# Kernel tuning notes

Hardware: AMD Instinct MI355X
Metric: run time of the kernel (lower is better)

## Reference

```python
import jax, jax.numpy as jnp
import numpy as np

D = 512
EPS = 1e-5  # torch BatchNorm1d default eps


def swish(x):
    return x * jax.nn.sigmoid(x)


def batchnorm_train(x, gamma, beta):
    # BatchNorm1d in training mode: biased batch stats
    m = jnp.mean(x, axis=0)
    v = jnp.mean((x - m) ** 2, axis=0)
    return gamma * (x - m) / jnp.sqrt(v + EPS) + beta


def setup_inputs() -> dict:
    key = jax.random.key(0)
    k_fea, k_w1, k_w2, k_lerp = jax.random.split(key, 4)
    bs, P = 32768, 8192
    fea = jax.random.normal(k_fea, (bs, D), dtype=jnp.float32)
    # first P rows are the minority (positive) class
    lbl = jnp.concatenate([jnp.ones((P, 1), jnp.int32), jnp.zeros((bs - P, 1), jnp.int32)], axis=0)
    scale = 1.0 / np.sqrt(D)
    W1 = jax.random.normal(k_w1, (D, D), dtype=jnp.float32) * scale
    W2 = jax.random.normal(k_w2, (D, D), dtype=jnp.float32) * scale
    b1 = jnp.zeros((D,), jnp.float32)
    b2 = jnp.zeros((D,), jnp.float32)
    g1 = jnp.ones((D,), jnp.float32)
    g2 = jnp.ones((D,), jnp.float32)
    beta1 = jnp.zeros((D,), jnp.float32)
    beta2 = jnp.zeros((D,), jnp.float32)
    lerp_w = jax.random.uniform(k_lerp, (P, 3), dtype=jnp.float32)
    return dict(fea=fea, lbl=lbl, W1=W1, b1=b1, g1=g1, beta1=beta1,
                W2=W2, b2=b2, g2=g2, beta2=beta2, lerp_w=lerp_w, num_pos=P)


def reference(fea, lbl, W1, b1, g1, beta1, W2, b2, g2, beta2, lerp_w, num_pos):
    # fea_transform: Linear -> BN -> Swish -> Linear -> BN -> Swish
    h = swish(batchnorm_train(fea @ W1 + b1, g1, beta1))
    h = swish(batchnorm_train(h @ W2 + b2, g2, beta2))

    # SMOTE path (training mode): KNN over positive-class features
    pos_idx = jnp.nonzero(lbl[:, 0] > 0, size=num_pos)[0]  # static-size gather
    x = h[pos_idx]                                          # (P, D)
    sq = jnp.sum(x * x, axis=-1)                            # (P,)
    # negative squared pairwise distance; topk largest == nearest
    neg_dist = 2.0 * (x @ x.T) - sq[:, None] - sq[None, :]  # (P, P)
    _, idx = jax.lax.top_k(neg_dist, 3)                     # (P, 3), idx[:,0] == self

    a = x[idx[:, 0]]                                        # (P, D) anchor
    b = x[idx]                                              # (P, 3, D) neighbors
    # torch.lerp(a, b, w) = a + w * (b - a), one random w per (i, j)
    new_fea = a[:, None, :] + lerp_w[..., None] * (b - a[:, None, :])
    new_fea = new_fea.reshape(-1, D)                        # (3P, D), row-major matches i,j loop order

    fea_out = jnp.concatenate([h, new_fea], axis=0)
    lbl_out = jnp.concatenate([lbl, jnp.ones((new_fea.shape[0], 1), lbl.dtype)], axis=0)
    return fea_out, lbl_out
```

## Files before the change

### kernel.cpp

```cpp
#include <hip/hip_runtime.h>
#include <math.h>

#define NEG_INF -3.402823466e38f
#define NSPLIT 8

typedef __attribute__((ext_vector_type(8))) short bf16x8;
typedef __attribute__((ext_vector_type(4))) float f32x4;

__device__ __forceinline__ void gload_lds16(const unsigned short* g, unsigned short* l) {
  __builtin_amdgcn_global_load_lds(
      (const __attribute__((address_space(1))) unsigned int*)g,
      (__attribute__((address_space(3))) unsigned int*)l, 16, 0, 0);
}
__device__ __forceinline__ void gload_lds16f(const float* g, float* l) {
  __builtin_amdgcn_global_load_lds(
      (const __attribute__((address_space(1))) unsigned int*)g,
      (__attribute__((address_space(3))) unsigned int*)l, 16, 0, 0);
}

__device__ __forceinline__ unsigned short f2bf(float f) {
  union { float f; unsigned int u; } a; a.f = f;
  unsigned int u = a.u;
  return (unsigned short)((u + 0x7fffu + ((u >> 16) & 1u)) >> 16);
}

__device__ __forceinline__ void split3_8(f32x4 a, f32x4 b,
                                         bf16x8& hi, bf16x8& md, bf16x8& lo) {
  union { bf16x8 v; unsigned int u[4]; } H, M, L;
  float f[8];
  f[0]=a[0]; f[1]=a[1]; f[2]=a[2]; f[3]=a[3];
  f[4]=b[0]; f[5]=b[1]; f[6]=b[2]; f[7]=b[3];
#pragma unroll
  for (int p = 0; p < 4; ++p) {
    union { float f; unsigned int u; } x0, x1, h0, h1, r0, r1, m0, m1, s0, s1;
    x0.f = f[2*p]; x1.f = f[2*p+1];
    H.u[p] = (x0.u >> 16) | (x1.u & 0xffff0000u);
    h0.u = x0.u & 0xffff0000u; h1.u = x1.u & 0xffff0000u;
    r0.f = x0.f - h0.f;        r1.f = x1.f - h1.f;
    M.u[p] = (r0.u >> 16) | (r1.u & 0xffff0000u);
    m0.u = r0.u & 0xffff0000u; m1.u = r1.u & 0xffff0000u;
    s0.f = r0.f - m0.f;        s1.f = r1.f - m1.f;
    L.u[p] = (s0.u >> 16) | (s1.u & 0xffff0000u);
  }
  hi = H.v; md = M.v; lo = L.v;
}

__global__ __launch_bounds__(256) void split_w_t3(const float* __restrict__ W,
    unsigned short* __restrict__ Th, unsigned short* __restrict__ Tm,
    unsigned short* __restrict__ Tl)
{
  __shared__ float T[64][65];
  int k0 = blockIdx.x * 64, n0 = blockIdx.y * 64;
  int tid = threadIdx.x;
  int r = tid >> 4, c4 = (tid & 15) << 2;
#pragma unroll
  for (int p = 0; p < 4; ++p) {
    int row = r + p * 16;
    float4 v = *(const float4*)&W[(size_t)(k0 + row) * 512 + n0 + c4];
    T[c4 + 0][row] = v.x; T[c4 + 1][row] = v.y;
    T[c4 + 2][row] = v.z; T[c4 + 3][row] = v.w;
  }
  __syncthreads();
  int nr = tid >> 2, kc = (tid & 3) << 4;
#pragma unroll
  for (int u = 0; u < 16; ++u) {
    union { float f; unsigned int u; } x, h, rr, m, ss;
    x.f = T[nr][kc + u];
    unsigned short hb = (unsigned short)(x.u >> 16);
    h.u = x.u & 0xffff0000u;
    rr.f = x.f - h.f;
    unsigned short mb = (unsigned short)(rr.u >> 16);
    m.u = rr.u & 0xffff0000u;
    ss.f = rr.f - m.f;
    unsigned short lb = (unsigned short)(ss.u >> 16);
    size_t o = (size_t)(n0 + nr) * 512 + k0 + kc + u;
    Th[o] = hb; Tm[o] = mb; Tl[o] = lb;
  }
}

__global__ __launch_bounds__(256, 2) void gemm_split3(
    const float* __restrict__ A, const unsigned short* __restrict__ Bth,
    const unsigned short* __restrict__ Btm, const unsigned short* __restrict__ Btl,
    const float* __restrict__ bias, float* __restrict__ C, float* __restrict__ partial)
{
  __shared__ char smem[81920];
  const int tid = threadIdx.x;
  const int w = tid >> 6, lane = tid & 63;
  const int wr = w >> 1, wc = w & 1;
  const int bm = blockIdx.x * 128, bn = blockIdx.y * 128;
  const int fr = lane & 15, fg = lane >> 4;
  const int arow = tid >> 3, acb = (tid & 7) << 4;
  const int brow = tid >> 2, bcb = (tid & 3) << 4;

  f32x4 acc[4][4];
#pragma unroll
  for (int mi = 0; mi < 4; ++mi)
#pragma unroll
    for (int ni = 0; ni < 4; ++ni) acc[mi][ni] = (f32x4){0.f, 0.f, 0.f, 0.f};

  auto STAGE = [&](int buf, int ktf) {
    float* sA = (float*)(smem + buf * 40960);
    unsigned short* sBh = (unsigned short*)(smem + buf * 40960 + 16384);
    unsigned short* sBm = sBh + 4096;
    unsigned short* sBl = sBm + 4096;
#pragma unroll
    for (int p = 0; p < 4; ++p) {
      int row = arow + p * 32;
      int cb = acb ^ ((row & 7) << 4);
      gload_lds16f(&A[(size_t)(bm + row) * 512 + ktf + (cb >> 2)],
                   &sA[row * 32 + (acb >> 2)]);
    }
#pragma unroll
    for (int p = 0; p < 2; ++p) {
      int row = brow + p * 64;
      int cb = bcb ^ (((row >> 1) & 3) << 4);
      int so = row * 32 + (bcb >> 1);
      gload_lds16(&Bth[(size_t)(bn + row) * 512 + ktf + (cb >> 1)], &sBh[so]);
      gload_lds16(&Btm[(size_t)(bn + row) * 512 + ktf + (cb >> 1)], &sBm[so]);
      gload_lds16(&Btl[(size_t)(bn + row) * 512 + ktf + (cb >> 1)], &sBl[so]);
    }
  };

  STAGE(0, 0);
  __syncthreads();
  for (int it = 0; it < 16; ++it) {
    int cur = it & 1;
    if (it + 1 < 16) STAGE(cur ^ 1, (it + 1) * 32);
    float* sA = (float*)(smem + cur * 40960);
    unsigned short* sBh = (unsigned short*)(smem + cur * 40960 + 16384);
    unsigned short* sBm = sBh + 4096;
    unsigned short* sBl = sBm + 4096;
    bf16x8 bh[4], bmf[4], blf[4];
#pragma unroll
    for (int ni = 0; ni < 4; ++ni) {
      int row = wc * 64 + ni * 16 + fr;
      int off = row * 32 + (((fg * 16) ^ (((row >> 1) & 3) << 4)) >> 1);
      bh[ni]  = *(const bf16x8*)&sBh[off];
      bmf[ni] = *(const bf16x8*)&sBm[off];
      blf[ni] = *(const bf16x8*)&sBl[off];
    }
    bf16x8 ah[4], am[4], al[4];
#pragma unroll
    for (int mi = 0; mi < 4; ++mi) {
      int row = wr * 64 + mi * 16 + fr;
      int swz = (row & 7) << 4;
      const char* rb = (const char*)(sA + row * 32);
      f32x4 f0 = *(const f32x4*)(rb + ((fg * 32) ^ swz));
      f32x4 f1 = *(const f32x4*)(rb + ((fg * 32 + 16) ^ swz));
      split3_8(f0, f1, ah[mi], am[mi], al[mi]);
    }
#pragma unroll
    for (int mi = 0; mi < 4; ++mi)
#pragma unroll
      for (int ni = 0; ni < 4; ++ni) {
        acc[mi][ni] = __builtin_amdgcn_mfma_f32_16x16x32_bf16(al[mi], bh[ni],  acc[mi][ni], 0, 0, 0);
        acc[mi][ni] = __builtin_amdgcn_mfma_f32_16x16x32_bf16(am[mi], bmf[ni], acc[mi][ni], 0, 0, 0);
        acc[mi][ni] = __builtin_amdgcn_mfma_f32_16x16x32_bf16(ah[mi], blf[ni], acc[mi][ni], 0, 0, 0);
        acc[mi][ni] = __builtin_amdgcn_mfma_f32_16x16x32_bf16(am[mi], bh[ni],  acc[mi][ni], 0, 0, 0);
        acc[mi][ni] = __builtin_amdgcn_mfma_f32_16x16x32_bf16(ah[mi], bmf[ni], acc[mi][ni], 0, 0, 0);
        acc[mi][ni] = __builtin_amdgcn_mfma_f32_16x16x32_bf16(ah[mi], bh[ni],  acc[mi][ni], 0, 0, 0);
      }
    __syncthreads();
  }
  float bno[4], s[4] = {0, 0, 0, 0}, q[4] = {0, 0, 0, 0};
#pragma unroll
  for (int ni = 0; ni < 4; ++ni) bno[ni] = bias[bn + wc * 64 + ni * 16 + fr];
#pragma unroll
  for (int mi = 0; mi < 4; ++mi) {
    int row = bm + wr * 64 + mi * 16 + fg * 4;
#pragma unroll
    for (int ni = 0; ni < 4; ++ni) {
      int col = bn + wc * 64 + ni * 16 + fr;
#pragma unroll
      for (int r = 0; r < 4; ++r) {
        float v = acc[mi][ni][r] + bno[ni];
        C[(size_t)(row + r) * 512 + col] = v;
        s[ni] += v; q[ni] += v * v;
      }
    }
  }
#pragma unroll
  for (int ni = 0; ni < 4; ++ni) {
    float ss = s[ni], qq = q[ni];
    ss += __shfl_xor(ss, 16); ss += __shfl_xor(ss, 32);
    qq += __shfl_xor(qq, 16); qq += __shfl_xor(qq, 32);
    if (fg == 0) {
      int slot = blockIdx.x * 2 + wr;
      int col = bn + wc * 64 + ni * 16 + fr;
      partial[(size_t)(slot * 2 + 0) * 512 + col] = ss;
      partial[(size_t)(slot * 2 + 1) * 512 + col] = qq;
    }
  }
}

__global__ __launch_bounds__(256) void bn_reduce1(
    const float* __restrict__ partial, float* __restrict__ partial2, int nslot)
{
  int g = blockIdx.x, p = blockIdx.y;
  int per = nslot >> 4;
  int t = threadIdx.x;
#pragma unroll
  for (int cc = 0; cc < 2; ++cc) {
    int c = t + cc * 256;
    float s = 0.f;
    for (int s0 = 0; s0 < per; ++s0) {
      int slot = g * per + s0;
      s += partial[(size_t)(slot * 2 + p) * 512 + c];
    }
    partial2[(size_t)(g * 2 + p) * 512 + c] = s;
  }
}

__global__ void bn_finalize(
    const float* __restrict__ partial2, const float* __restrict__ g,
    const float* __restrict__ beta, float* __restrict__ scale,
    float* __restrict__ shift, int rows)
{
  int c = blockIdx.x * blockDim.x + threadIdx.x;
  if (c >= 512) return;
  float s = 0, s2 = 0;
  for (int b = 0; b < 16; ++b) {
    s  += partial2[(size_t)(b * 2 + 0) * 512 + c];
    s2 += partial2[(size_t)(b * 2 + 1) * 512 + c];
  }
  float m = s / rows;
  float v = s2 / rows - m * m;
  if (v < 0) v = 0;
  float sc = g[c] / sqrtf(v + 1e-5f);
  scale[c] = sc;
  shift[c] = beta[c] - m * sc;
}

__global__ void bn_swish(
    const float* __restrict__ Y, const float* __restrict__ scale,
    const float* __restrict__ shift, float* __restrict__ H, int total4)
{
  int i = blockIdx.x * blockDim.x + threadIdx.x;
  if (i >= total4) return;
  float4 y = ((const float4*)Y)[i];
  int c = (i * 4) & 511;
  float z;
  float4 o;
  z = y.x * scale[c + 0] + shift[c + 0]; o.x = z / (1.f + expf(-z));
  z = y.y * scale[c + 1] + shift[c + 1]; o.y = z / (1.f + expf(-z));
  z = y.z * scale[c + 2] + shift[c + 2]; o.z = z / (1.f + expf(-z));
  z = y.w * scale[c + 3] + shift[c + 3]; o.w = z / (1.f + expf(-z));
  ((float4*)H)[i] = o;
}

__global__ __launch_bounds__(1024) void pos_count(const int* __restrict__ lbl, int n,
                                                  int* __restrict__ cnt,
                                                  int* __restrict__ pos, int P)
{
  int b = blockIdx.x, tid = threadIdx.x;
  int i = b * 1024 + tid;
  if (i < P) pos[i] = 0;
  int pred = (i < n) && (lbl[i] > 0);
  unsigned long long m = __ballot(pred);
  __shared__ int ws[16];
  if ((tid & 63) == 0) ws[tid >> 6] = __popcll(m);
  __syncthreads();
  if (tid == 0) { int s = 0; for (int k = 0; k < 16; ++k) s += ws[k]; cnt[b] = s; }
}

__global__ void pos_prefix(int* __restrict__ cnt, int nb)
{
  if (threadIdx.x == 0) {
    int s = 0;
    for (int b = 0; b < nb; ++b) { int c = cnt[b]; cnt[b] = s; s += c; }
  }
}

__global__ __launch_bounds__(1024) void pos_scatter(const int* __restrict__ lbl, int n,
                                                    const int* __restrict__ cntp,
                                                    int* __restrict__ pos, int P)
{
  int b = blockIdx.x, tid = threadIdx.x;
  int i = b * 1024 + tid;
  int pred = (i < n) && (lbl[i] > 0);
  unsigned long long m = __ballot(pred);
  __shared__ int ws[16];
  int wid = tid >> 6, lane = tid & 63;
  if (lane == 0) ws[wid] = __popcll(m);
  __syncthreads();
  int wbase = 0;
  for (int w2 = 0; w2 < wid; ++w2) wbase += ws[w2];
  int rank = cntp[b] + wbase + __popcll(m & ((1ull << lane) - 1ull));
  if (pred && rank < P) pos[rank] = i;
}

__global__ void gather_sq(const float* __restrict__ H, const int* __restrict__ pos,
                          float* __restrict__ X, unsigned short* __restrict__ Xh,
                          float* __restrict__ sq)
{
  int r = blockIdx.x, t = threadIdx.x;
  int src = pos[r];
  float4 v = *(const float4*)&H[src * 512 + t * 4];
  *(float4*)&X[r * 512 + t * 4] = v;
  ushort4 hv;
  hv.x = f2bf(v.x); hv.y = f2bf(v.y); hv.z = f2bf(v.z); hv.w = f2bf(v.w);
  *(ushort4*)&Xh[r * 512 + t * 4] = hv;
  float s = v.x * v.x + v.y * v.y + v.z * v.z + v.w * v.w;
#pragma unroll
  for (int off = 32; off > 0; off >>= 1) s += __shfl_down(s, off);
  __shared__ float red[2];
  if ((t & 63) == 0) red[t >> 6] = s;
  __syncthreads();
  if (t == 0) sq[r] = red[0] + red[1];
}

__global__ __launch_bounds__(256, 2) void gram8(
    const unsigned short* __restrict__ Xh, const float* __restrict__ sq, int P,
    float* __restrict__ p8v, int* __restrict__ p8j)
{
  __shared__ char smem[65536];
  __shared__ float sqj_l[2][128];

  const int tid = threadIdx.x;
  const int w = tid >> 6, lane = tid & 63;
  const int ih = w >> 1, jh = w & 1;
  const int bi = blockIdx.x * 128;
  const int jchunk = P / NSPLIT;
  const int jlo = blockIdx.y * jchunk;
  const int ntile = jchunk >> 7;
  const int total = ntile * 8;

  const int srow = tid >> 3;
  const int scb = (tid & 7) << 4;
  const int fr = lane & 15, fg = lane >> 4;

  float t8[4][8]; int j8[4][8];
#pragma unroll
  for (int mi = 0; mi < 4; ++mi)
#pragma unroll
    for (int q = 0; q < 8; ++q) { t8[mi][q] = NEG_INF; j8[mi][q] = 0x7fffffff; }

  auto STAGE = [&](int s) {
    int kt = (s & 7) << 6;
    int j0 = jlo + ((s >> 3) << 7);
    unsigned short* bA = (unsigned short*)(smem + ((s & 1) << 15));
    unsigned short* bB = bA + 8192;
#pragma unroll
    for (int it = 0; it < 4; ++it) {
      int row = srow + it * 32;
      int cb = scb ^ ((row & 7) << 4);
      gload_lds16(&Xh[(size_t)(bi + row) * 512 + kt + (cb >> 1)], &bA[row * 64 + (scb >> 1)]);
      gload_lds16(&Xh[(size_t)(j0 + row) * 512 + kt + (cb >> 1)], &bB[row * 64 + (scb >> 1)]);
    }
  };

  STAGE(0);
  if (tid < 128) sqj_l[0][tid] = sq[jlo + tid];
  __syncthreads();

  f32x4 acc[4][4];
  for (int s = 0; s < total; ++s) {
    if ((s & 7) == 0) {
#pragma unroll
      for (int a = 0; a < 4; ++a)
#pragma unroll
        for (int b = 0; b < 4; ++b) acc[a][b] = (f32x4){0.f, 0.f, 0.f, 0.f};
    }
    if (s + 1 < total) {
      STAGE(s + 1);
      if (((s + 1) & 7) == 0) {
        int jt1 = (s + 1) >> 3;
        if (tid < 128) sqj_l[jt1 & 1][tid] = sq[jlo + (jt1 << 7) + tid];
      }
    }
    unsigned short* bA = (unsigned short*)(smem + ((s & 1) << 15));
    unsigned short* bB = bA + 8192;
#pragma unroll
    for (int ks = 0; ks < 2; ++ks) {
      bf16x8 af[4], bfr[4];
      int kb = ks * 64 + fg * 16;
#pragma unroll
      for (int mi = 0; mi < 4; ++mi) {
        int row = ih * 64 + mi * 16 + fr;
        af[mi] = *(const bf16x8*)&bA[row * 64 + ((kb ^ ((row & 7) << 4)) >> 1)];
      }
#pragma unroll
      for (int nj = 0; nj < 4; ++nj) {
        int row = jh * 64 + nj * 16 + fr;
        bfr[nj] = *(const bf16x8*)&bB[row * 64 + ((kb ^ ((row & 7) << 4)) >> 1)];
      }
#pragma unroll
      for (int nj = 0; nj < 4; ++nj)
#pragma unroll
        for (int mi = 0; mi < 4; ++mi)
          acc[nj][mi] = __builtin_amdgcn_mfma_f32_16x16x32_bf16(
              bfr[nj], af[mi], acc[nj][mi], 0, 0, 0);
    }
    if ((s & 7) == 7) {
      int jt = s >> 3;
      int j0 = jlo + (jt << 7);
      int par = jt & 1;
#pragma unroll
      for (int nj = 0; nj < 4; ++nj) {
        f32x4 sv = *(const f32x4*)&sqj_l[par][jh * 64 + nj * 16 + fg * 4];
        int jb = j0 + jh * 64 + nj * 16 + fg * 4;
#pragma unroll
        for (int mi = 0; mi < 4; ++mi) {
#pragma unroll
          for (int r = 0; r < 4; ++r) {
            float v = 2.0f * acc[nj][mi][r] - sv[r];
            if (v > t8[mi][7]) {
              t8[mi][7] = v; j8[mi][7] = jb + r;
#pragma unroll
              for (int q = 7; q > 0; --q)
                if (t8[mi][q] > t8[mi][q - 1]) {
                  float tv = t8[mi][q]; t8[mi][q] = t8[mi][q - 1]; t8[mi][q - 1] = tv;
                  int tj = j8[mi][q]; j8[mi][q] = j8[mi][q - 1]; j8[mi][q - 1] = tj;
                }
            }
          }
        }
      }
    }
    __syncthreads();
  }

  float* mv = (float*)smem;
  int* mj = (int*)(smem + 32768);
#pragma unroll
  for (int mi = 0; mi < 4; ++mi)
#pragma unroll
    for (int q = 0; q < 8; ++q) {
      int idx = ((w * 4 + mi) * 16 + fr) * 32 + fg * 8 + q;
      mv[idx] = t8[mi][q]; mj[idx] = j8[mi][q];
    }
  __syncthreads();
  {
    int mi = lane >> 4, cc = lane & 15;
    int base = ((w * 4 + mi) * 16 + cc) * 32;
    int h0 = 0, h1 = 0, h2 = 0, h3 = 0;
    int i = bi + ih * 64 + mi * 16 + cc;
    int set = blockIdx.y * 2 + jh;
    size_t ob = ((size_t)i * (NSPLIT * 2) + set) * 8;
    for (int k = 0; k < 8; ++k) {
      float bv = NEG_INF; int bj = 0x7fffffff; int bg = 0;
      { float v = mv[base + h0];      int jj = mj[base + h0];      if (h0 < 8 && (v > bv || (v == bv && jj < bj))) { bv = v; bj = jj; bg = 0; } }
      { float v = mv[base + 8 + h1];  int jj = mj[base + 8 + h1];  if (h1 < 8 && (v > bv || (v == bv && jj < bj))) { bv = v; bj = jj; bg = 1; } }
      { float v = mv[base + 16 + h2]; int jj = mj[base + 16 + h2]; if (h2 < 8 && (v > bv || (v == bv && jj < bj))) { bv = v; bj = jj; bg = 2; } }
      { float v = mv[base + 24 + h3]; int jj = mj[base + 24 + h3]; if (h3 < 8 && (v > bv || (v == bv && jj < bj))) { bv = v; bj = jj; bg = 3; } }
      h0 += (bg == 0); h1 += (bg == 1); h2 += (bg == 2); h3 += (bg == 3);
      p8v[ob + k] = bv; p8j[ob + k] = bj;
    }
  }
}

__global__ void merge8(const float* __restrict__ p8v, const int* __restrict__ p8j,
                       int* __restrict__ cand, int P)
{
  int i = blockIdx.x * blockDim.x + threadIdx.x;
  if (i >= P) return;
  const int S = NSPLIT * 2;
  int head[S];
#pragma unroll
  for (int s = 0; s < S; ++s) head[s] = 0;
  const float* v = p8v + (size_t)i * S * 8;
  const int* j = p8j + (size_t)i * S * 8;
  for (int k = 0; k < 8; ++k) {
    float bv = NEG_INF; int bj = 0x7fffffff; int bs = 0;
#pragma unroll
    for (int s = 0; s < S; ++s) {
      if (head[s] < 8) {
        float vv = v[s * 8 + head[s]];
        int jj = j[s * 8 + head[s]];
        if (vv > bv || (vv == bv && jj < bj)) { bv = vv; bj = jj; bs = s; }
      }
    }
    head[bs]++;
    cand[i * 8 + k] = bj;
  }
}

__global__ __launch_bounds__(64) void rescore(
    const float* __restrict__ X, const float* __restrict__ sq,
    const int* __restrict__ cand, int* __restrict__ idx3)
{
  int i = blockIdx.x;
  int lane = threadIdx.x;
  f32x4 x0 = *(const f32x4*)&X[(size_t)i * 512 + lane * 8];
  f32x4 x1 = *(const f32x4*)&X[(size_t)i * 512 + lane * 8 + 4];
  float d[8]; int cj[8];
#pragma unroll
  for (int c = 0; c < 8; ++c) {
    int j = cand[i * 8 + c];
    cj[c] = j;
    f32x4 y0 = *(const f32x4*)&X[(size_t)j * 512 + lane * 8];
    f32x4 y1 = *(const f32x4*)&X[(size_t)j * 512 + lane * 8 + 4];
    float p = x0.x * y0.x + x0.y * y0.y + x0.z * y0.z + x0.w * y0.w
            + x1.x * y1.x + x1.y * y1.y + x1.z * y1.z + x1.w * y1.w;
#pragma unroll
    for (int off = 32; off > 0; off >>= 1) p += __shfl_xor(p, off);
    d[c] = 2.0f * p - sq[i] - sq[j];
  }
  if (lane == 0) {
    for (int k = 0; k < 3; ++k) {
      int b = 0;
#pragma unroll
      for (int c = 1; c < 8; ++c)
        if (d[c] > d[b] || (d[c] == d[b] && cj[c] < cj[b])) b = c;
      idx3[i * 3 + k] = cj[b];
      d[b] = NEG_INF; cj[b] = 0x7fffffff;
    }
  }
}

__global__ void make_newfea(const float* __restrict__ X, const int* __restrict__ idx3,
                            const float* __restrict__ lw, float* __restrict__ out)
{
  int r = blockIdx.x;
  int i = r / 3, k = r - i * 3;
  int ai = idx3[i * 3 + 0];
  int bi = idx3[i * 3 + k];
  float w = lw[r];
  int t = threadIdx.x;
  float4 av = *(const float4*)&X[ai * 512 + t * 4];
  float4 bv = *(const float4*)&X[bi * 512 + t * 4];
  float4 o;
  o.x = av.x + w * (bv.x - av.x);
  o.y = av.y + w * (bv.y - av.y);
  o.z = av.z + w * (bv.z - av.z);
  o.w = av.w + w * (bv.w - av.w);
  *(float4*)&out[(size_t)r * 512 + t * 4] = o;
}

__global__ void write_lbl(const int* __restrict__ lbl, float* __restrict__ out,
                          int n_in, int n_total)
{
  int i = blockIdx.x * blockDim.x + threadIdx.x;
  if (i < n_total) out[i] = (i < n_in) ? (float)lbl[i] : 1.0f;
}

extern "C" void kernel_launch(void* const* d_in, const int* in_sizes, int n_in,
                              void* d_out, int out_size, void* d_ws, size_t ws_size,
                              hipStream_t stream)
{
  const float* fea   = (const float*)d_in[0];
  const int*   lbl   = (const int*)d_in[1];
  const float* W1    = (const float*)d_in[2];
  const float* b1    = (const float*)d_in[3];
  const float* g1    = (const float*)d_in[4];
  const float* beta1 = (const float*)d_in[5];
  const float* W2    = (const float*)d_in[6];
  const float* b2    = (const float*)d_in[7];
  const float* g2    = (const float*)d_in[8];
  const float* beta2 = (const float*)d_in[9];
  const float* lerp_w = (const float*)d_in[10];

  int bs = in_sizes[0] / 512;
  int P  = in_sizes[10] / 3;
  int n_total = bs + 3 * P;

  float* out_f = (float*)d_out;
  float* Hout = out_f;
  float* newfea = out_f + (size_t)bs * 512;
  float* lbl_out = out_f + (size_t)n_total * 512;

  const size_t MB = 1024 * 1024;
  const size_t KB = 1024;
  char* ws = (char*)d_ws;
  float* Y1 = (float*)ws;
  float* X  = (float*)(ws + 64 * MB);
  unsigned short* W1h = (unsigned short*)(ws + 64 * MB);
  unsigned short* W1m = (unsigned short*)(ws + 64 * MB + 512 * KB);
  unsigned short* W1l = (unsigned short*)(ws + 64 * MB + 1024 * KB);
  unsigned short* W2h = (unsigned short*)(ws + 64 * MB + 1536 * KB);
  unsigned short* W2m = (unsigned short*)(ws + 64 * MB + 2048 * KB);
  unsigned short* W2l = (unsigned short*)(ws + 64 * MB + 2560 * KB);
  float* partial = (float*)(ws + 80 * MB);
  float* scale = (float*)(ws + 82 * MB);
  float* shiftv = scale + 512;
  float* sq = shiftv + 512;
  int* pos = (int*)(sq + 8192);
  int* idx3 = pos + 8192;
  int* cnt = idx3 + 3 * 8192;
  float* partial2 = (float*)(ws + 83 * MB);
  unsigned short* Xh = (unsigned short*)ws;
  float* p8v = (float*)(ws + 8 * MB);
  int*   p8j = (int*)(ws + 12 * MB);
  int*   cand = (int*)(ws + 16 * MB);

  dim3 wgrid(8, 8);
  split_w_t3<<<wgrid, 256, 0, stream>>>(W1, W1h, W1m, W1l);
  split_w_t3<<<wgrid, 256, 0, stream>>>(W2, W2h, W2m, W2l);

  dim3 ggrid(bs / 128, 4);
  int nslot = (bs / 128) * 2;
  dim3 rgrid(16, 2);

  gemm_split3<<<ggrid, 256, 0, stream>>>(fea, W1h, W1m, W1l, b1, Y1, partial);
  bn_reduce1<<<rgrid, 256, 0, stream>>>(partial, partial2, nslot);
  bn_finalize<<<2, 256, 0, stream>>>(partial2, g1, beta1, scale, shiftv, bs);
  bn_swish<<<(bs * 512 / 4 + 255) / 256, 256, 0, stream>>>(Y1, scale, shiftv, Y1, bs * 512 / 4);

  gemm_split3<<<ggrid, 256, 0, stream>>>(Y1, W2h, W2m, W2l, b2, Hout, partial);
  bn_reduce1<<<rgrid, 256, 0, stream>>>(partial, partial2, nslot);
  bn_finalize<<<2, 256, 0, stream>>>(partial2, g2, beta2, scale, shiftv, bs);
  bn_swish<<<(bs * 512 / 4 + 255) / 256, 256, 0, stream>>>(Hout, scale, shiftv, Hout, bs * 512 / 4);

  int nb = (bs + 1023) / 1024;
  pos_count<<<nb, 1024, 0, stream>>>(lbl, bs, cnt, pos, P);
  pos_prefix<<<1, 64, 0, stream>>>(cnt, nb);
  pos_scatter<<<nb, 1024, 0, stream>>>(lbl, bs, cnt, pos, P);
  gather_sq<<<P, 128, 0, stream>>>(Hout, pos, X, Xh, sq);

  dim3 gram_grid(P / 128, NSPLIT);
  gram8<<<gram_grid, 256, 0, stream>>>(Xh, sq, P, p8v, p8j);
  merge8<<<(P + 255) / 256, 256, 0, stream>>>(p8v, p8j, cand, P);
  rescore<<<P, 64, 0, stream>>>(X, sq, cand, idx3);

  make_newfea<<<3 * P, 128, 0, stream>>>(X, idx3, lerp_w, newfea);
  write_lbl<<<(n_total + 255) / 256, 256, 0, stream>>>(lbl, lbl_out, bs, n_total);
}
```

Baseline: 536.5 us.

## Rewrite gram8 with single-buffered tiles, LDS transpose for per-row top-8, NSPLIT 16

The Gram/top-k kernel drops its double-buffered global-to-LDS pipeline and now loads each K slice synchronously. The distance tile is staged through an LDS buffer so each lane keeps a single top-8 list for one query row, which replaces the per-fragment lists and the in-block 4-way merge. NSPLIT doubles to 16 for more blocks, with the partial buffers spaced further apart to fit. The costs are lost load/compute overlap, extra barriers per tile, a serial 16-step insertion per lane, and twice as many partial lists for the merge kernel.

Measured after the change: 529.7 us. About the same (-1.3%).

```diff
diff --git a/kernel.cpp b/kernel.cpp
--- a/kernel.cpp
+++ b/kernel.cpp
@@ -2,7 +2,7 @@
 #include <math.h>
 
 #define NEG_INF -3.402823466e38f
-#define NSPLIT 8
+#define NSPLIT 16
 
 typedef __attribute__((ext_vector_type(8))) short bf16x8;
 typedef __attribute__((ext_vector_type(4))) float f32x4;
@@ -313,140 +313,102 @@
     const unsigned short* __restrict__ Xh, const float* __restrict__ sq, int P,
     float* __restrict__ p8v, int* __restrict__ p8j)
 {
-  __shared__ char smem[65536];
-  __shared__ float sqj_l[2][128];
+  __shared__ unsigned short Ah[128 * 64];
+  __shared__ unsigned short Bh[128 * 64];
+  __shared__ float dl[4][64][17];
+  __shared__ float sqj_l[128];
 
   const int tid = threadIdx.x;
   const int w = tid >> 6, lane = tid & 63;
-  const int ih = w >> 1, jh = w & 1;
+  const int wr = w >> 1, wc = w & 1;
   const int bi = blockIdx.x * 128;
   const int jchunk = P / NSPLIT;
   const int jlo = blockIdx.y * jchunk;
-  const int ntile = jchunk >> 7;
-  const int total = ntile * 8;
 
   const int srow = tid >> 3;
-  const int scb = (tid & 7) << 4;
+  const int scb  = (tid & 7) << 4;
   const int fr = lane & 15, fg = lane >> 4;
 
-  float t8[4][8]; int j8[4][8];
-#pragma unroll
-  for (int mi = 0; mi < 4; ++mi)
-#pragma unroll
-    for (int q = 0; q < 8; ++q) { t8[mi][q] = NEG_INF; j8[mi][q] = 0x7fffffff; }
-
-  auto STAGE = [&](int s) {
-    int kt = (s & 7) << 6;
-    int j0 = jlo + ((s >> 3) << 7);
-    unsigned short* bA = (unsigned short*)(smem + ((s & 1) << 15));
-    unsigned short* bB = bA + 8192;
-#pragma unroll
-    for (int it = 0; it < 4; ++it) {
-      int row = srow + it * 32;
-      int cb = scb ^ ((row & 7) << 4);
-      gload_lds16(&Xh[(size_t)(bi + row) * 512 + kt + (cb >> 1)], &bA[row * 64 + (scb >> 1)]);
-      gload_lds16(&Xh[(size_t)(j0 + row) * 512 + kt + (cb >> 1)], &bB[row * 64 + (scb >> 1)]);
-    }
-  };
-
-  STAGE(0);
-  if (tid < 128) sqj_l[0][tid] = sq[jlo + tid];
-  __syncthreads();
-
-  f32x4 acc[4][4];
-  for (int s = 0; s < total; ++s) {
-    if ((s & 7) == 0) {
-#pragma unroll
-      for (int a = 0; a < 4; ++a)
-#pragma unroll
-        for (int b = 0; b < 4; ++b) acc[a][b] = (f32x4){0.f, 0.f, 0.f, 0.f};
-    }
-    if (s + 1 < total) {
-      STAGE(s + 1);
-      if (((s + 1) & 7) == 0) {
-        int jt1 = (s + 1) >> 3;
-        if (tid < 128) sqj_l[jt1 & 1][tid] = sq[jlo + (jt1 << 7) + tid];
+  float t[8]; int ji[8];
+#pragma unroll
+  for (int q = 0; q < 8; ++q) { t[q] = NEG_INF; ji[q] = 0x7fffffff; }
+
+  for (int jt = 0; jt < jchunk; jt += 128) {
+    const int j0 = jlo + jt;
+    if (tid < 128) sqj_l[tid] = sq[j0 + tid];
+    f32x4 acc[4][4];
+#pragma unroll
+    for (int mi = 0; mi < 4; ++mi)
+#pragma unroll
+      for (int ni = 0; ni < 4; ++ni) acc[mi][ni] = (f32x4){0.f, 0.f, 0.f, 0.f};
+
+    for (int kt = 0; kt < 512; kt += 64) {
+#pragma unroll
+      for (int it = 0; it < 4; ++it) {
+        int row = srow + it * 32;
+        int cb = scb ^ ((row & 7) << 4);
+        gload_lds16(&Xh[(size_t)(bi + row) * 512 + kt + (cb >> 1)],
+                    &Ah[row * 64 + (scb >> 1)]);
+        gload_lds16(&Xh[(size_t)(j0 + row) * 512 + kt + (cb >> 1)],
+                    &Bh[row * 64 + (scb >> 1)]);
       }
-    }
-    unsigned short* bA = (unsigned short*)(smem + ((s & 1) << 15));
-    unsigned short* bB = bA + 8192;
-#pragma unroll
-    for (int ks = 0; ks < 2; ++ks) {
-      bf16x8 af[4], bfr[4];
-      int kb = ks * 64 + fg * 16;
-#pragma unroll
-      for (int mi = 0; mi < 4; ++mi) {
-        int row = ih * 64 + mi * 16 + fr;
-        af[mi] = *(const bf16x8*)&bA[row * 64 + ((kb ^ ((row & 7) << 4)) >> 1)];
+      __syncthreads();
+#pragma unroll
+      for (int ks = 0; ks < 2; ++ks) {
+        bf16x8 af[4], bfr[4];
+        int kb = ks * 64 + fg * 16;
+#pragma unroll
+        for (int mi = 0; mi < 4; ++mi) {
+          int row = wr * 64 + mi * 16 + fr;
+          af[mi] = *(const bf16x8*)&Ah[row * 64 + ((kb ^ ((row & 7) << 4)) >> 1)];
+        }
+#pragma unroll
+        for (int ni = 0; ni < 4; ++ni) {
+          int row = wc * 64 + ni * 16 + fr;
+          bfr[ni] = *(const bf16x8*)&Bh[row * 64 + ((kb ^ ((row & 7) << 4)) >> 1)];
+        }
+#pragma unroll
+        for (int mi = 0; mi < 4; ++mi)
+#pragma unroll
+          for (int ni = 0; ni < 4; ++ni)
+            acc[mi][ni] = __builtin_amdgcn_mfma_f32_16x16x32_bf16(
+                af[mi], bfr[ni], acc[mi][ni], 0, 0, 0);
       }
-#pragma unroll
-      for (int nj = 0; nj < 4; ++nj) {
-        int row = jh * 64 + nj * 16 + fr;
-        bfr[nj] = *(const bf16x8*)&bB[row * 64 + ((kb ^ ((row & 7) << 4)) >> 1)];
-      }
-#pragma unroll
-      for (int nj = 0; nj < 4; ++nj)
-#pragma unroll
-        for (int mi = 0; mi < 4; ++mi)
-          acc[nj][mi] = __builtin_amdgcn_mfma_f32_16x16x32_bf16(
-              bfr[nj], af[mi], acc[nj][mi], 0, 0, 0);
-    }
-    if ((s & 7) == 7) {
-      int jt = s >> 3;
-      int j0 = jlo + (jt << 7);
-      int par = jt & 1;
-#pragma unroll
-      for (int nj = 0; nj < 4; ++nj) {
-        f32x4 sv = *(const f32x4*)&sqj_l[par][jh * 64 + nj * 16 + fg * 4];
-        int jb = j0 + jh * 64 + nj * 16 + fg * 4;
-#pragma unroll
-        for (int mi = 0; mi < 4; ++mi) {
-#pragma unroll
-          for (int r = 0; r < 4; ++r) {
-            float v = 2.0f * acc[nj][mi][r] - sv[r];
-            if (v > t8[mi][7]) {
-              t8[mi][7] = v; j8[mi][7] = jb + r;
-#pragma unroll
-              for (int q = 7; q > 0; --q)
-                if (t8[mi][q] > t8[mi][q - 1]) {
-                  float tv = t8[mi][q]; t8[mi][q] = t8[mi][q - 1]; t8[mi][q - 1] = tv;
-                  int tj = j8[mi][q]; j8[mi][q] = j8[mi][q - 1]; j8[mi][q - 1] = tj;
-                }
+      __syncthreads();
+    }
+
+#pragma unroll
+    for (int qn = 0; qn < 4; ++qn) {
+      float sqv = sqj_l[wc * 64 + qn * 16 + fr];
+#pragma unroll
+      for (int mi = 0; mi < 4; ++mi)
+#pragma unroll
+        for (int r = 0; r < 4; ++r)
+          dl[w][mi * 16 + fg * 4 + r][fr] = 2.0f * acc[mi][qn][r] - sqv;
+      __syncthreads();
+      int jbase = j0 + wc * 64 + qn * 16;
+      for (int c = 0; c < 16; ++c) {
+        float v = dl[w][lane][c];
+        if (v > t[7]) {
+          t[7] = v; ji[7] = jbase + c;
+#pragma unroll
+          for (int q = 7; q > 0; --q) {
+            if (t[q] > t[q - 1]) {
+              float tv = t[q]; t[q] = t[q - 1]; t[q - 1] = tv;
+              int tj = ji[q]; ji[q] = ji[q - 1]; ji[q - 1] = tj;
             }
           }
         }
       }
-    }
-    __syncthreads();
-  }
-
-  float* mv = (float*)smem;
-  int* mj = (int*)(smem + 32768);
-#pragma unroll
-  for (int mi = 0; mi < 4; ++mi)
-#pragma unroll
-    for (int q = 0; q < 8; ++q) {
-      int idx = ((w * 4 + mi) * 16 + fr) * 32 + fg * 8 + q;
-      mv[idx] = t8[mi][q]; mj[idx] = j8[mi][q];
-    }
-  __syncthreads();
-  {
-    int mi = lane >> 4, cc = lane & 15;
-    int base = ((w * 4 + mi) * 16 + cc) * 32;
-    int h0 = 0, h1 = 0, h2 = 0, h3 = 0;
-    int i = bi + ih * 64 + mi * 16 + cc;
-    int set = blockIdx.y * 2 + jh;
-    size_t ob = ((size_t)i * (NSPLIT * 2) + set) * 8;
-    for (int k = 0; k < 8; ++k) {
-      float bv = NEG_INF; int bj = 0x7fffffff; int bg = 0;
-      { float v = mv[base + h0];      int jj = mj[base + h0];      if (h0 < 8 && (v > bv || (v == bv && jj < bj))) { bv = v; bj = jj; bg = 0; } }
-      { float v = mv[base + 8 + h1];  int jj = mj[base + 8 + h1];  if (h1 < 8 && (v > bv || (v == bv && jj < bj))) { bv = v; bj = jj; bg = 1; } }
-      { float v = mv[base + 16 + h2]; int jj = mj[base + 16 + h2]; if (h2 < 8 && (v > bv || (v == bv && jj < bj))) { bv = v; bj = jj; bg = 2; } }
-      { float v = mv[base + 24 + h3]; int jj = mj[base + 24 + h3]; if (h3 < 8 && (v > bv || (v == bv && jj < bj))) { bv = v; bj = jj; bg = 3; } }
-      h0 += (bg == 0); h1 += (bg == 1); h2 += (bg == 2); h3 += (bg == 3);
-      p8v[ob + k] = bv; p8j[ob + k] = bj;
-    }
-  }
+      __syncthreads();
+    }
+  }
+
+  int row = bi + wr * 64 + lane;
+  int set = blockIdx.y * 2 + wc;
+  size_t base = ((size_t)row * (NSPLIT * 2) + set) * 8;
+#pragma unroll
+  for (int q = 0; q < 8; ++q) { p8v[base + q] = t[q]; p8j[base + q] = ji[q]; }
 }
 
 __global__ void merge8(const float* __restrict__ p8v, const int* __restrict__ p8j,
@@ -580,8 +542,8 @@
   float* partial2 = (float*)(ws + 83 * MB);
   unsigned short* Xh = (unsigned short*)ws;
   float* p8v = (float*)(ws + 8 * MB);
-  int*   p8j = (int*)(ws + 12 * MB);
-  int*   cand = (int*)(ws + 16 * MB);
+  int*   p8j = (int*)(ws + 16 * MB);
+  int*   cand = (int*)(ws + 24 * MB);
 
   dim3 wgrid(8, 8);
   split_w_t3<<<wgrid, 256, 0, stream>>>(W1, W1h, W1m, W1l);
```
